# Performance work log

Hardware: AMD Instinct MI355X
Metric: run time of the kernel (lower is better)

Reference implementation:

```python
import jax, jax.numpy as jnp
import numpy as np


def setup_inputs() -> dict:
    key = jax.random.key(0)
    ks = jax.random.split(key, 6)
    B, N, Cd, Qd, E, G = 256, 196, 2048, 1024, 1024, 8
    s = lambda d: 1.0 / np.sqrt(d)
    return {
        "context": jax.random.normal(ks[0], (B, N, Cd), dtype=jnp.float32),
        "query": jax.random.normal(ks[1], (B, Qd), dtype=jnp.float32),
        "Wq": jax.random.normal(ks[2], (E, Qd), dtype=jnp.float32) * s(Qd),
        "bq": jnp.zeros((E,), dtype=jnp.float32),
        "Wc": jax.random.normal(ks[3], (E, Cd), dtype=jnp.float32) * s(Cd),
        "bc": jnp.zeros((E,), dtype=jnp.float32),
        "Wo": jax.random.normal(ks[4], (G, E), dtype=jnp.float32) * s(E),
        "bo": jnp.zeros((G,), dtype=jnp.float32),
    }


def reference(context, query, Wq, bq, Wc, bc, Wo, bo):
    # query: [B, Qd] -> [B, 1, E]; context: [B, N, Cd] -> [B, N, E]
    qp = (query @ Wq.T + bq)[:, None, :]
    cp = jnp.einsum('bnc,ec->bne', context, Wc) + bc
    # dropout in eval mode (identity)
    combined = jnp.tanh(qp + cp)                      # [B, N, E]
    attn = jnp.einsum('bne,ge->bng', combined, Wo) + bo  # [B, N, G]
    weights = jax.nn.softmax(attn, axis=1)            # softmax over regions
    glimpses = jnp.einsum('bng,bnc->bgc', weights, context)  # [B, G, Cd]
    return glimpses.reshape(context.shape[0], -1)     # [B, G*Cd]
```

## Files before the change

kernel.cpp:

```cpp
#include <hip/hip_runtime.h>
#include <stdint.h>

typedef unsigned int u32;
typedef __bf16 bf16_t;
typedef bf16_t bf16x8 __attribute__((ext_vector_type(8)));
typedef bf16_t bf16x4 __attribute__((ext_vector_type(4)));
typedef float  f32x4  __attribute__((ext_vector_type(4)));

#define NB   256
#define NN   196
#define CD   2048
#define QD   1024
#define NE   1024
#define NG   8

#define WS_QP    0
#define WS_ATTN  (NB*NE*4)
#define WS_WCB   (WS_ATTN + NB*NG*NN*4)

__device__ __forceinline__ bf16_t f2bf(float f){
  u32 u = __float_as_uint(f);
  u += 0x7fffu + ((u >> 16) & 1u);
  unsigned short h = (unsigned short)(u >> 16);
  return __builtin_bit_cast(bf16_t, h);
}

__device__ __forceinline__ float fast_tanh(float x){
  float e = __expf(2.0f * x);
  return 1.0f - 2.0f / (e + 1.0f);
}

__device__ __forceinline__ void load_lds16(const void* g, void* l){
  __builtin_amdgcn_global_load_lds(
      (const __attribute__((address_space(1))) void*)g,
      (__attribute__((address_space(3))) void*)l, 16, 0, 0);
}

__global__ __launch_bounds__(256)
void k_conv(const float* __restrict__ src, bf16_t* __restrict__ dst){
  size_t i = ((size_t)blockIdx.x * 256 + threadIdx.x) * 4;
  float4 v = *(const float4*)(src + i);
  bf16x4 o = { f2bf(v.x), f2bf(v.y), f2bf(v.z), f2bf(v.w) };
  *(bf16x4*)(dst + i) = o;
}

__global__ __launch_bounds__(256)
void k_qp(const float* __restrict__ query, const float* __restrict__ Wq,
          const float* __restrict__ bq, float* __restrict__ qp){
  __shared__ float qs[32][36];
  __shared__ float wsm[32][36];
  const u32 t  = threadIdx.x;
  const u32 e0 = blockIdx.x * 32, b0 = blockIdx.y * 32;
  const u32 r  = t >> 3, ci = (t & 7) * 4;
  const u32 tm = (t >> 4) * 2, tn = (t & 15) * 2;
  float c00 = 0.f, c01 = 0.f, c10 = 0.f, c11 = 0.f;
  for (u32 k0 = 0; k0 < QD; k0 += 32){
    float4 qv = *(const float4*)(query + (size_t)(b0 + r) * QD + k0 + ci);
    float4 wv = *(const float4*)(Wq    + (size_t)(e0 + r) * QD + k0 + ci);
    __syncthreads();
    *(float4*)&qs[r][ci]  = qv;
    *(float4*)&wsm[r][ci] = wv;
    __syncthreads();
    #pragma unroll
    for (int kq = 0; kq < 8; kq++){
      float4 a0 = *(const float4*)&qs[tm][kq*4];
      float4 a1 = *(const float4*)&qs[tm+1][kq*4];
      float4 b0v = *(const float4*)&wsm[tn][kq*4];
      float4 b1v = *(const float4*)&wsm[tn+1][kq*4];
      c00 += a0.x*b0v.x + a0.y*b0v.y + a0.z*b0v.z + a0.w*b0v.w;
      c01 += a0.x*b1v.x + a0.y*b1v.y + a0.z*b1v.z + a0.w*b1v.w;
      c10 += a1.x*b0v.x + a1.y*b0v.y + a1.z*b0v.z + a1.w*b0v.w;
      c11 += a1.x*b1v.x + a1.y*b1v.y + a1.z*b1v.z + a1.w*b1v.w;
    }
  }
  float bq0 = bq[e0+tn], bq1 = bq[e0+tn+1];
  qp[(size_t)(b0+tm  )*NE + e0+tn  ] = c00 + bq0;
  qp[(size_t)(b0+tm  )*NE + e0+tn+1] = c01 + bq1;
  qp[(size_t)(b0+tm+1)*NE + e0+tn  ] = c10 + bq0;
  qp[(size_t)(b0+tm+1)*NE + e0+tn+1] = c11 + bq1;
}

#define BM 128
#define BN 128
#define BK 32
#define KSTEPS (CD/BK)

__global__ __launch_bounds__(256, 2)
void k_mainf(const float* __restrict__ ctx, const bf16_t* __restrict__ wcb,
             const float* __restrict__ qp, const float* __restrict__ bcv,
             const float* __restrict__ Wo, float* __restrict__ attn)
{
  __shared__ char smem[36864] __attribute__((aligned(128)));

  const u32 tid  = threadIdx.x;
  const u32 lane = tid & 63;
  const u32 wave = tid >> 6;
  const u32 wm   = wave >> 1;
  const u32 wn   = wave & 1;

  u32 d  = blockIdx.x;
  u32 x  = d & 7;
  u32 s  = d >> 3;
  u32 ec = s & 7;
  u32 j  = s >> 3;
  u32 ms = j * 8 + x;
  const u32 m0 = ms * BM;
  const u32 e0 = ec * BN;

  const u32 arow = tid >> 1;
  const u32 ah   = tid & 1;
  const u32 asw  = (arow >> 1) & 3;
  const u32 ap0  = ((ah*2 + 0) ^ asw) * 16;
  const u32 ap1  = ((ah*2 + 1) ^ asw) * 16;
  const float* aSrc = ctx + (size_t)(m0 + arow) * CD + ah * 16;

  const u32 brow0 = tid >> 2;
  const u32 brow1 = (tid + 256) >> 2;
  const u32 bkq0  = (tid & 3) ^ ((tid >> 3) & 3);
  const u32 bkq1  = (tid & 3) ^ (((tid + 256) >> 3) & 3);
  const bf16_t* bS0 = wcb + (size_t)(e0 + brow0) * CD + bkq0 * 8;
  const bf16_t* bS1 = wcb + (size_t)(e0 + brow1) * CD + bkq1 * 8;
  char* bD0 = smem + 16384 + tid * 16;
  char* bD1 = bD0 + 4096;

  f32x4 acc[4][4];
  #pragma unroll
  for (int i = 0; i < 4; i++)
    #pragma unroll
    for (int jn = 0; jn < 4; jn++) acc[i][jn] = (f32x4){0.f,0.f,0.f,0.f};

  float4 av[4];
  auto issueA = [&](u32 ks){
    const float* p = aSrc + ks * BK;
    av[0] = *(const float4*)(p);
    av[1] = *(const float4*)(p + 4);
    av[2] = *(const float4*)(p + 8);
    av[3] = *(const float4*)(p + 12);
  };
  auto stageB = [&](u32 buf, u32 ks){
    load_lds16(bS0 + ks * BK, bD0 + buf * 8192u);
    load_lds16(bS1 + ks * BK, bD1 + buf * 8192u);
  };
  auto writeA = [&](u32 buf){
    bf16x8 lo = { (bf16_t)av[0].x, (bf16_t)av[0].y, (bf16_t)av[0].z, (bf16_t)av[0].w,
                  (bf16_t)av[1].x, (bf16_t)av[1].y, (bf16_t)av[1].z, (bf16_t)av[1].w };
    bf16x8 hi = { (bf16_t)av[2].x, (bf16_t)av[2].y, (bf16_t)av[2].z, (bf16_t)av[2].w,
                  (bf16_t)av[3].x, (bf16_t)av[3].y, (bf16_t)av[3].z, (bf16_t)av[3].w };
    char* base = smem + buf * 8192u + arow * 64u;
    *(bf16x8*)(base + ap0) = lo;
    *(bf16x8*)(base + ap1) = hi;
  };

  const u32 q   = lane >> 4;
  const u32 r15 = lane & 15;
  const u32 sw  = (q ^ ((r15 >> 1) & 3)) * 16;

  auto compute = [&](u32 buf){
    const char* A = smem + buf * 8192u;
    const char* B = smem + 16384u + buf * 8192u;
    bf16x8 af[4], bfr[4];
    #pragma unroll
    for (int mt = 0; mt < 4; mt++){
      u32 row = wm*64 + mt*16 + r15;
      af[mt] = *(const bf16x8*)(A + row*64 + sw);
    }
    #pragma unroll
    for (int nt = 0; nt < 4; nt++){
      u32 row = wn*64 + nt*16 + r15;
      bfr[nt] = *(const bf16x8*)(B + row*64 + sw);
    }
    #pragma unroll
    for (int mt = 0; mt < 4; mt++)
      #pragma unroll
      for (int nt = 0; nt < 4; nt++)
        acc[mt][nt] = __builtin_amdgcn_mfma_f32_16x16x32_bf16(af[mt], bfr[nt], acc[mt][nt], 0, 0, 0);
  };

  issueA(0);
  stageB(0, 0);
  writeA(0);
  __syncthreads();

  for (u32 kt = 0; kt < KSTEPS; kt++){
    if (kt + 1 < KSTEPS){
      issueA(kt + 1);
      stageB((kt + 1) & 1, kt + 1);
    }
    compute(kt & 1);
    if (kt + 1 < KSTEPS)
      writeA((kt + 1) & 1);
    __syncthreads();
  }

  float*  qp0  = (float*)(smem + 34816);
  float*  qp1  = (float*)(smem + 35328);
  float*  bcs  = (float*)(smem + 35840);
  bf16_t* comb = (bf16_t*)smem;

  const u32 b0  = m0 / 196u;
  const u32 bnd = (b0 + 1) * 196u - m0;

  if (tid < 128){
    qp0[tid] = qp[(size_t)b0 * NE + e0 + tid];
    bcs[tid] = bcv[e0 + tid];
  } else {
    u32 b1 = b0 + 1; if (b1 >= NB) b1 = NB - 1;
    qp1[tid - 128] = qp[(size_t)b1 * NE + e0 + (tid - 128)];
  }

  bf16x8 wf[4];
  {
    u32 g = lane & 15;
    #pragma unroll
    for (int kk = 0; kk < 4; kk++){
      #pragma unroll
      for (int rr = 0; rr < 8; rr++){
        u32 ei = e0 + kk*32 + q*8 + rr;
        float v = (g < NG) ? Wo[(size_t)g * NE + ei] : 0.0f;
        wf[kk][rr] = f2bf(v);
      }
    }
  }
  __syncthreads();

  #pragma unroll
  for (int nt = 0; nt < 4; nt++){
    u32 el = wn*64 + nt*16 + r15;
    float qa = qp0[el];
    float qb = qp1[el];
    float bcx = bcs[el];
    #pragma unroll
    for (int mt = 0; mt < 4; mt++){
      u32 rl = wm*64 + mt*16 + q*4;
      #pragma unroll
      for (int r = 0; r < 4; r++){
        u32 row = rl + r;
        float qv = (row >= bnd) ? qb : qa;
        float t = fast_tanh(acc[mt][nt][r] + qv + bcx);
        comb[row*136 + el] = f2bf(t);
      }
    }
  }
  __syncthreads();

  #pragma unroll
  for (int i = 0; i < 2; i++){
    u32 nrow = (wave*2 + i)*16 + r15;
    f32x4 at = (f32x4){0.f,0.f,0.f,0.f};
    #pragma unroll
    for (int kk = 0; kk < 4; kk++){
      bf16x8 cf = *(const bf16x8*)&comb[nrow*136 + kk*32 + q*8];
      at = __builtin_amdgcn_mfma_f32_16x16x32_bf16(wf[kk], cf, at, 0, 0, 0);
    }
    if (q < 2){
      u32 mrow = m0 + nrow;
      u32 bb = mrow / 196u;
      u32 nn = mrow - bb * 196u;
      #pragma unroll
      for (int r = 0; r < 4; r++){
        u32 g = q*4 + r;
        atomicAdd(&attn[((size_t)bb * NG + g) * NN + nn], at[r]);
      }
    }
  }
}

__global__ __launch_bounds__(256)
void k_softmax(float* __restrict__ attn){
  u32 flat = blockIdx.x * 4 + (threadIdx.x >> 6);
  u32 lane = threadIdx.x & 63;
  float* row = attn + (size_t)flat * NN;
  float v0 = row[lane];
  float v1 = row[lane + 64];
  float v2 = row[lane + 128];
  float v3 = (lane < 4) ? row[lane + 192] : -1e30f;
  float m = fmaxf(fmaxf(v0, v1), fmaxf(v2, v3));
  #pragma unroll
  for (int o = 1; o < 64; o <<= 1) m = fmaxf(m, __shfl_xor(m, o));
  float e0 = __expf(v0 - m), e1 = __expf(v1 - m), e2 = __expf(v2 - m);
  float e3 = (lane < 4) ? __expf(v3 - m) : 0.f;
  float sum = e0 + e1 + e2 + e3;
  #pragma unroll
  for (int o = 1; o < 64; o <<= 1) sum += __shfl_xor(sum, o);
  float inv = 1.0f / sum;
  row[lane]       = e0 * inv;
  row[lane + 64]  = e1 * inv;
  row[lane + 128] = e2 * inv;
  if (lane < 4) row[lane + 192] = e3 * inv;
}

__global__ __launch_bounds__(256)
void k_glimpse(const float* __restrict__ ctx, const float* __restrict__ w,
               float* __restrict__ out){
  const u32 b  = blockIdx.y;
  const u32 c0 = blockIdx.x * 512 + threadIdx.x * 2;
  __shared__ float ws_[NG * NN];
  for (u32 i = threadIdx.x; i < NG * NN; i += 256)
    ws_[i] = w[(size_t)b * NG * NN + i];
  __syncthreads();
  const float* cp = ctx + (size_t)b * NN * CD + c0;
  float2 acc[NG];
  #pragma unroll
  for (int g = 0; g < NG; g++) acc[g] = make_float2(0.f, 0.f);
  for (u32 n = 0; n < NN; n++){
    float2 v = *(const float2*)(cp + (size_t)n * CD);
    #pragma unroll
    for (int g = 0; g < NG; g++){
      float wv = ws_[g * NN + n];
      acc[g].x = fmaf(wv, v.x, acc[g].x);
      acc[g].y = fmaf(wv, v.y, acc[g].y);
    }
  }
  #pragma unroll
  for (int g = 0; g < NG; g++)
    *(float2*)(out + (size_t)b * (NG * CD) + (size_t)g * CD + c0) = acc[g];
}

extern "C" void kernel_launch(void* const* d_in, const int* in_sizes, int n_in,
                              void* d_out, int out_size, void* d_ws, size_t ws_size,
                              hipStream_t stream)
{
  const float* ctx   = (const float*)d_in[0];
  const float* query = (const float*)d_in[1];
  const float* Wq    = (const float*)d_in[2];
  const float* bq    = (const float*)d_in[3];
  const float* Wc    = (const float*)d_in[4];
  const float* bc    = (const float*)d_in[5];
  const float* Wo    = (const float*)d_in[6];

  char* ws = (char*)d_ws;
  float*  qp   = (float*)(ws + WS_QP);
  float*  attn = (float*)(ws + WS_ATTN);
  bf16_t* wcb  = (bf16_t*)(ws + WS_WCB);
  float*  out  = (float*)d_out;

  (void)hipMemsetAsync(attn, 0, (size_t)NB * NG * NN * 4, stream);
  k_conv<<<2048, 256, 0, stream>>>(Wc, wcb);
  k_qp<<<dim3(32, 8), 256, 0, stream>>>(query, Wq, bq, qp);
  k_mainf<<<3136, 256, 0, stream>>>(ctx, wcb, qp, bc, Wo, attn);
  k_softmax<<<512, 256, 0, stream>>>(attn);
  k_glimpse<<<dim3(4, 256), 256, 0, stream>>>(ctx, attn, out);
}
```

Before: 511.8 us.

## Stage fp32 context tiles directly to LDS via async loads, convert at fragment read

After: 480.5 us (median of 3 runs). 6.1% less time.

```diff
diff --git a/kernel.cpp b/kernel.cpp
--- a/kernel.cpp
+++ b/kernel.cpp
@@ -85,12 +85,12 @@
 #define BK 32
 #define KSTEPS (CD/BK)
 
-__global__ __launch_bounds__(256, 2)
-void k_mainf(const float* __restrict__ ctx, const bf16_t* __restrict__ wcb,
+__global__ __launch_bounds__(256, 3)
+void k_mainA(const float* __restrict__ ctx, const bf16_t* __restrict__ wcb,
              const float* __restrict__ qp, const float* __restrict__ bcv,
              const float* __restrict__ Wo, float* __restrict__ attn)
 {
-  __shared__ char smem[36864] __attribute__((aligned(128)));
+  __shared__ char smem[49152] __attribute__((aligned(128)));
 
   const u32 tid  = threadIdx.x;
   const u32 lane = tid & 63;
@@ -107,12 +107,10 @@
   const u32 m0 = ms * BM;
   const u32 e0 = ec * BN;
 
-  const u32 arow = tid >> 1;
-  const u32 ah   = tid & 1;
-  const u32 asw  = (arow >> 1) & 3;
-  const u32 ap0  = ((ah*2 + 0) ^ asw) * 16;
-  const u32 ap1  = ((ah*2 + 1) ^ asw) * 16;
-  const float* aSrc = ctx + (size_t)(m0 + arow) * CD + ah * 16;
+  const u32 arow = tid >> 3;
+  const u32 aq   = (tid & 7) ^ (arow & 7);
+  const float* aS = ctx + (size_t)(m0 + arow) * CD + aq * 4;
+  char* aD = smem + tid * 16;
 
   const u32 brow0 = tid >> 2;
   const u32 brow1 = (tid + 256) >> 2;
@@ -120,7 +118,7 @@
   const u32 bkq1  = (tid & 3) ^ (((tid + 256) >> 3) & 3);
   const bf16_t* bS0 = wcb + (size_t)(e0 + brow0) * CD + bkq0 * 8;
   const bf16_t* bS1 = wcb + (size_t)(e0 + brow1) * CD + bkq1 * 8;
-  char* bD0 = smem + 16384 + tid * 16;
+  char* bD0 = smem + 32768 + tid * 16;
   char* bD1 = bD0 + 4096;
 
   f32x4 acc[4][4];
@@ -129,45 +127,39 @@
     #pragma unroll
     for (int jn = 0; jn < 4; jn++) acc[i][jn] = (f32x4){0.f,0.f,0.f,0.f};
 
-  float4 av[4];
-  auto issueA = [&](u32 ks){
-    const float* p = aSrc + ks * BK;
-    av[0] = *(const float4*)(p);
-    av[1] = *(const float4*)(p + 4);
-    av[2] = *(const float4*)(p + 8);
-    av[3] = *(const float4*)(p + 12);
-  };
-  auto stageB = [&](u32 buf, u32 ks){
-    load_lds16(bS0 + ks * BK, bD0 + buf * 8192u);
-    load_lds16(bS1 + ks * BK, bD1 + buf * 8192u);
-  };
-  auto writeA = [&](u32 buf){
-    bf16x8 lo = { (bf16_t)av[0].x, (bf16_t)av[0].y, (bf16_t)av[0].z, (bf16_t)av[0].w,
-                  (bf16_t)av[1].x, (bf16_t)av[1].y, (bf16_t)av[1].z, (bf16_t)av[1].w };
-    bf16x8 hi = { (bf16_t)av[2].x, (bf16_t)av[2].y, (bf16_t)av[2].z, (bf16_t)av[2].w,
-                  (bf16_t)av[3].x, (bf16_t)av[3].y, (bf16_t)av[3].z, (bf16_t)av[3].w };
-    char* base = smem + buf * 8192u + arow * 64u;
-    *(bf16x8*)(base + ap0) = lo;
-    *(bf16x8*)(base + ap1) = hi;
+  auto stage = [&](u32 buf, u32 ks){
+    const u32 ko = ks * BK;
+    #pragma unroll
+    for (int p = 0; p < 4; p++)
+      load_lds16(aS + (size_t)(p * 32) * CD + ko, aD + buf * 16384u + p * 4096u);
+    load_lds16(bS0 + ko, bD0 + buf * 8192u);
+    load_lds16(bS1 + ko, bD1 + buf * 8192u);
   };
 
   const u32 q   = lane >> 4;
   const u32 r15 = lane & 15;
-  const u32 sw  = (q ^ ((r15 >> 1) & 3)) * 16;
+  const u32 as0 = ((2*q)     ^ (r15 & 7)) * 16;
+  const u32 as1 = ((2*q + 1) ^ (r15 & 7)) * 16;
+  const u32 bsw = (q ^ ((r15 >> 1) & 3)) * 16;
 
   auto compute = [&](u32 buf){
-    const char* A = smem + buf * 8192u;
-    const char* B = smem + 16384u + buf * 8192u;
+    const char* A = smem + buf * 16384u;
+    const char* B = smem + 32768u + buf * 8192u;
     bf16x8 af[4], bfr[4];
     #pragma unroll
     for (int mt = 0; mt < 4; mt++){
       u32 row = wm*64 + mt*16 + r15;
-      af[mt] = *(const bf16x8*)(A + row*64 + sw);
+      const char* rb = A + row * 128u;
+      f32x4 lo = *(const f32x4*)(rb + as0);
+      f32x4 hi = *(const f32x4*)(rb + as1);
+      bf16x8 v = { (bf16_t)lo[0], (bf16_t)lo[1], (bf16_t)lo[2], (bf16_t)lo[3],
+                   (bf16_t)hi[0], (bf16_t)hi[1], (bf16_t)hi[2], (bf16_t)hi[3] };
+      af[mt] = v;
     }
     #pragma unroll
     for (int nt = 0; nt < 4; nt++){
       u32 row = wn*64 + nt*16 + r15;
-      bfr[nt] = *(const bf16x8*)(B + row*64 + sw);
+      bfr[nt] = *(const bf16x8*)(B + row*64 + bsw);
     }
     #pragma unroll
     for (int mt = 0; mt < 4; mt++)
@@ -176,25 +168,17 @@
         acc[mt][nt] = __builtin_amdgcn_mfma_f32_16x16x32_bf16(af[mt], bfr[nt], acc[mt][nt], 0, 0, 0);
   };
 
-  issueA(0);
-  stageB(0, 0);
-  writeA(0);
+  stage(0, 0);
   __syncthreads();
-
-  for (u32 kt = 0; kt < KSTEPS; kt++){
-    if (kt + 1 < KSTEPS){
-      issueA(kt + 1);
-      stageB((kt + 1) & 1, kt + 1);
-    }
-    compute(kt & 1);
-    if (kt + 1 < KSTEPS)
-      writeA((kt + 1) & 1);
+  for (u32 ks = 0; ks < KSTEPS; ks++){
+    if (ks + 1 < KSTEPS) stage((ks + 1) & 1, ks + 1);
+    compute(ks & 1);
     __syncthreads();
   }
 
-  float*  qp0  = (float*)(smem + 34816);
-  float*  qp1  = (float*)(smem + 35328);
-  float*  bcs  = (float*)(smem + 35840);
+  float*  qp0  = (float*)(smem + 35840);
+  float*  qp1  = (float*)(smem + 36352);
+  float*  bcs  = (float*)(smem + 36864);
   bf16_t* comb = (bf16_t*)smem;
 
   const u32 b0  = m0 / 196u;
@@ -337,7 +321,7 @@
   (void)hipMemsetAsync(attn, 0, (size_t)NB * NG * NN * 4, stream);
   k_conv<<<2048, 256, 0, stream>>>(Wc, wcb);
   k_qp<<<dim3(32, 8), 256, 0, stream>>>(query, Wq, bq, qp);
-  k_mainf<<<3136, 256, 0, stream>>>(ctx, wcb, qp, bc, Wo, attn);
+  k_mainA<<<3136, 256, 0, stream>>>(ctx, wcb, qp, bc, Wo, attn);
   k_softmax<<<512, 256, 0, stream>>>(attn);
   k_glimpse<<<dim3(4, 256), 256, 0, stream>>>(ctx, attn, out);
 }
```
